# Optimization experiments

Measured on AMD Instinct MI355X. Metric: run time of the kernel, lower is better.

## Reference

```python
import jax, jax.numpy as jnp
import numpy as np

EPS = 1e-8

def _cdist(a, b):
    # Euclidean pairwise distances, torch.cdist(p=2) equivalent.
    sq = (jnp.sum(a * a, axis=1)[:, None] + jnp.sum(b * b, axis=1)[None, :]
          - 2.0 * (a @ b.T))
    return jnp.sqrt(jnp.maximum(sq, 1e-12))

def setup_inputs() -> dict:
    key = jax.random.key(0)
    k1, k2, k3, k4, k5, k6 = jax.random.split(key, 6)
    ns, n_cls, n_feat, K = 4096, 500, 256, 400
    return {
        "src_x": jax.random.normal(k1, (ns, n_feat), dtype=jnp.float32),
        "tgt_x": jax.random.normal(k2, (ns, n_feat), dtype=jnp.float32),
        "src_y": jax.random.uniform(k3, (ns, n_cls), dtype=jnp.float32),
        "tgt_y": jax.random.uniform(k4, (ns, n_cls), dtype=jnp.float32),
        "queue": jax.random.normal(k5, (n_cls, n_feat, K), dtype=jnp.float32),
        "queue_size": jax.random.randint(k6, (n_cls,), 0, K, dtype=jnp.int32),
    }

def reference(src_x, tgt_x, src_y, tgt_y, queue, queue_size):
    n_cls, n_feat, K = queue.shape
    num = queue_size.astype(queue.dtype)[:, None]                      # (C,1)
    # src_centroid: masked mean over the first queue_size[c] columns
    valid = (jnp.arange(K)[None, :] < queue_size[:, None]).astype(queue.dtype)  # (C,K)
    centroid = jnp.einsum('cfk,ck->cf', queue, valid) / jnp.maximum(num, 1.0)
    centroid = jnp.where(num > 0, centroid, 0.0)                       # (C,F)

    batch_src = src_y.T @ src_x                                        # (C,F)
    total_num = num + jnp.sum(src_y, axis=0)[:, None] + EPS            # (C,1)
    mean_src = (centroid * num + batch_src) / total_num                # (C,F)

    batch_prob = jnp.sum(tgt_y, axis=0)[:, None] + EPS                 # (C,1)
    mean_tgt = (tgt_y.T @ tgt_x) / batch_prob                          # (C,F)

    intra = jnp.diagonal(_cdist(mean_src, mean_tgt)).mean()
    inter = _cdist(mean_src, mean_src).mean()
    return intra, inter
```

## Files before the change

kernel.cpp:

```cpp
#include <hip/hip_runtime.h>
#include <math.h>

#define NS 4096
#define NC 500
#define NF 256
#define NK 400
#define KC_GEMM 16
#define NQB 4000

__global__ __launch_bounds__(256, 4) void k_heavy(
    const float* __restrict__ Xs, const float* __restrict__ Ys, float* __restrict__ Ps,
    const float* __restrict__ Xt, const float* __restrict__ Yt, float* __restrict__ Pt,
    float* __restrict__ CSs, float* __restrict__ CSt,
    const float* __restrict__ queue, const int* __restrict__ qsize,
    float* __restrict__ qsum) {
  __shared__ float ytile[256][16];
  __shared__ float csbuf[256];
  const int b    = blockIdx.x;
  const int tid  = threadIdx.x;
  const int w    = tid >> 6;
  const int lane = tid & 63;
  const int hp   = b % 5;

  for (int it = 0; it < 5; ++it) {
    if (it == hp) {
      const int z  = b >> 9;
      const int kc = (b >> 5) & 15;
      const int c0 = (b & 31) * 16;
      const float* X = z ? Xt : Xs;
      const float* Y = z ? Yt : Ys;
      float*       P = z ? Pt : Ps;
      float*      CS = z ? CSt : CSs;
      const int n0   = kc * 256;
      const int cmax = (NC - c0 < 16) ? (NC - c0) : 16;

      float csum = 0.f;
      for (int i = tid; i < 256 * 16; i += 256) {
        int rr = i >> 4, cc = i & 15;
        float v = (cc < cmax) ? Y[(size_t)(n0 + rr) * NC + c0 + cc] : 0.f;
        ytile[rr][cc] = v;
        csum += v;
      }
      csbuf[tid] = csum;
      __syncthreads();

      float acc[16];
      #pragma unroll
      for (int j = 0; j < 16; ++j) acc[j] = 0.f;
      const float* Xp = X + (size_t)n0 * NF + tid;

      #pragma unroll 4
      for (int n = 0; n < 256; ++n) {
        float xv = Xp[(size_t)n * NF];
        float4 y0 = *reinterpret_cast<const float4*>(&ytile[n][0]);
        float4 y1 = *reinterpret_cast<const float4*>(&ytile[n][4]);
        float4 y2 = *reinterpret_cast<const float4*>(&ytile[n][8]);
        float4 y3 = *reinterpret_cast<const float4*>(&ytile[n][12]);
        acc[0]  = fmaf(y0.x, xv, acc[0]);  acc[1]  = fmaf(y0.y, xv, acc[1]);
        acc[2]  = fmaf(y0.z, xv, acc[2]);  acc[3]  = fmaf(y0.w, xv, acc[3]);
        acc[4]  = fmaf(y1.x, xv, acc[4]);  acc[5]  = fmaf(y1.y, xv, acc[5]);
        acc[6]  = fmaf(y1.z, xv, acc[6]);  acc[7]  = fmaf(y1.w, xv, acc[7]);
        acc[8]  = fmaf(y2.x, xv, acc[8]);  acc[9]  = fmaf(y2.y, xv, acc[9]);
        acc[10] = fmaf(y2.z, xv, acc[10]); acc[11] = fmaf(y2.w, xv, acc[11]);
        acc[12] = fmaf(y3.x, xv, acc[12]); acc[13] = fmaf(y3.y, xv, acc[13]);
        acc[14] = fmaf(y3.z, xv, acc[14]); acc[15] = fmaf(y3.w, xv, acc[15]);
      }

      if (tid < 16) {
        float t = 0.f;
        #pragma unroll
        for (int j = 0; j < 16; ++j) t += csbuf[tid + 16 * j];
        CS[kc * 512 + c0 + tid] = t;
      }

      #pragma unroll
      for (int j = 0; j < 16; ++j)
        if (j < cmax) P[((size_t)kc * NC + c0 + j) * NF + tid] = acc[j];
      __syncthreads();

    } else {
      const int j = it - (it > hp ? 1 : 0);
      const int q = j * 1024 + b;
      if (q < NQB) {
        const int r0 = q * 32 + w * 8;
        const int c  = r0 >> 8;
        const int qs = qsize[c];
        const int L  = (qs + 3) >> 2;
        const float* base = queue + (size_t)r0 * NK;
        float s0 = 0.f, s1 = 0.f, s2 = 0.f, s3 = 0.f;
        float s4 = 0.f, s5 = 0.f, s6 = 0.f, s7 = 0.f;

        if (lane < L) {
          const int k = 4 * lane;
          float4 v0 = *reinterpret_cast<const float4*>(base + 0 * NK + k);
          float4 v1 = *reinterpret_cast<const float4*>(base + 1 * NK + k);
          float4 v2 = *reinterpret_cast<const float4*>(base + 2 * NK + k);
          float4 v3 = *reinterpret_cast<const float4*>(base + 3 * NK + k);
          float4 v4 = *reinterpret_cast<const float4*>(base + 4 * NK + k);
          float4 v5 = *reinterpret_cast<const float4*>(base + 5 * NK + k);
          float4 v6 = *reinterpret_cast<const float4*>(base + 6 * NK + k);
          float4 v7 = *reinterpret_cast<const float4*>(base + 7 * NK + k);
          s0 += v0.x; s1 += v1.x; s2 += v2.x; s3 += v3.x;
          s4 += v4.x; s5 += v5.x; s6 += v6.x; s7 += v7.x;
          if (k + 1 < qs) { s0 += v0.y; s1 += v1.y; s2 += v2.y; s3 += v3.y;
                            s4 += v4.y; s5 += v5.y; s6 += v6.y; s7 += v7.y; }
          if (k + 2 < qs) { s0 += v0.z; s1 += v1.z; s2 += v2.z; s3 += v3.z;
                            s4 += v4.z; s5 += v5.z; s6 += v6.z; s7 += v7.z; }
          if (k + 3 < qs) { s0 += v0.w; s1 += v1.w; s2 += v2.w; s3 += v3.w;
                            s4 += v4.w; s5 += v5.w; s6 += v6.w; s7 += v7.w; }
        }
        if (lane + 64 < L) {
          const int k = 256 + 4 * lane;
          float4 v0 = *reinterpret_cast<const float4*>(base + 0 * NK + k);
          float4 v1 = *reinterpret_cast<const float4*>(base + 1 * NK + k);
          float4 v2 = *reinterpret_cast<const float4*>(base + 2 * NK + k);
          float4 v3 = *reinterpret_cast<const float4*>(base + 3 * NK + k);
          float4 v4 = *reinterpret_cast<const float4*>(base + 4 * NK + k);
          float4 v5 = *reinterpret_cast<const float4*>(base + 5 * NK + k);
          float4 v6 = *reinterpret_cast<const float4*>(base + 6 * NK + k);
          float4 v7 = *reinterpret_cast<const float4*>(base + 7 * NK + k);
          s0 += v0.x; s1 += v1.x; s2 += v2.x; s3 += v3.x;
          s4 += v4.x; s5 += v5.x; s6 += v6.x; s7 += v7.x;
          if (k + 1 < qs) { s0 += v0.y; s1 += v1.y; s2 += v2.y; s3 += v3.y;
                            s4 += v4.y; s5 += v5.y; s6 += v6.y; s7 += v7.y; }
          if (k + 2 < qs) { s0 += v0.z; s1 += v1.z; s2 += v2.z; s3 += v3.z;
                            s4 += v4.z; s5 += v5.z; s6 += v6.z; s7 += v7.z; }
          if (k + 3 < qs) { s0 += v0.w; s1 += v1.w; s2 += v2.w; s3 += v3.w;
                            s4 += v4.w; s5 += v5.w; s6 += v6.w; s7 += v7.w; }
        }
        #pragma unroll
        for (int m = 32; m; m >>= 1) {
          s0 += __shfl_xor(s0, m); s1 += __shfl_xor(s1, m);
          s2 += __shfl_xor(s2, m); s3 += __shfl_xor(s3, m);
          s4 += __shfl_xor(s4, m); s5 += __shfl_xor(s5, m);
          s6 += __shfl_xor(s6, m); s7 += __shfl_xor(s7, m);
        }
        if (lane == 0) {
          *reinterpret_cast<float4*>(&qsum[r0])     = make_float4(s0, s1, s2, s3);
          *reinterpret_cast<float4*>(&qsum[r0 + 4]) = make_float4(s4, s5, s6, s7);
        }
      }
    }
  }
}

__global__ __launch_bounds__(256) void k_means(
    const float* __restrict__ qsum, const int* __restrict__ qsize,
    const float* __restrict__ Psrc, const float* __restrict__ Ptgt,
    const float* __restrict__ CSsrc, const float* __restrict__ CStgt,
    float* __restrict__ MS, float* __restrict__ MT, float* __restrict__ ipart) {
  const int c = blockIdx.x * 4 + (threadIdx.x >> 6);
  const int lane = threadIdx.x & 63;
  const int f4 = lane * 4;
  if (c >= NC) return;

  float cs_s = 0.f, cs_t = 0.f;
  #pragma unroll
  for (int kc = 0; kc < KC_GEMM; ++kc) {
    cs_s += CSsrc[kc * 512 + c];
    cs_t += CStgt[kc * 512 + c];
  }
  float num = (float)qsize[c];
  float4 ns = *reinterpret_cast<const float4*>(&qsum[(size_t)c * NF + f4]);
  float4 nt = make_float4(0.f, 0.f, 0.f, 0.f);
  #pragma unroll
  for (int kc = 0; kc < KC_GEMM; ++kc) {
    float4 ps = *reinterpret_cast<const float4*>(&Psrc[((size_t)kc * NC + c) * NF + f4]);
    float4 pt = *reinterpret_cast<const float4*>(&Ptgt[((size_t)kc * NC + c) * NF + f4]);
    ns.x += ps.x; ns.y += ps.y; ns.z += ps.z; ns.w += ps.w;
    nt.x += pt.x; nt.y += pt.y; nt.z += pt.z; nt.w += pt.w;
  }
  float rs = 1.f / (num + cs_s + 1e-8f);
  float rt = 1.f / (cs_t + 1e-8f);
  float4 ms = make_float4(ns.x * rs, ns.y * rs, ns.z * rs, ns.w * rs);
  float4 mt = make_float4(nt.x * rt, nt.y * rt, nt.z * rt, nt.w * rt);
  *reinterpret_cast<float4*>(&MS[(size_t)c * NF + f4]) = ms;
  *reinterpret_cast<float4*>(&MT[(size_t)c * NF + f4]) = mt;

  float dx = ms.x - mt.x, dy = ms.y - mt.y, dz = ms.z - mt.z, dw = ms.w - mt.w;
  float s = dx * dx + dy * dy + dz * dz + dw * dw;
  #pragma unroll
  for (int m = 32; m; m >>= 1) s += __shfl_xor(s, m);
  if (lane == 0) ipart[c] = sqrtf(fmaxf(s, 1e-12f));
}

#define TC 16
#define NBT 32
__global__ __launch_bounds__(256) void k_dist(const float* __restrict__ MS,
                                              float* __restrict__ epart) {
  __shared__ float a[TC][NF + 4];
  __shared__ float b[TC][NF + 4];
  const int bi = blockIdx.x & (NBT - 1);
  const int bj = blockIdx.x >> 5;

  for (int i = threadIdx.x; i < TC * (NF / 4); i += 256) {
    int rr = i >> 6, fq = (i & 63) * 4;
    int c1 = bi * TC + rr;
    int c2 = bj * TC + rr;
    float4 va = (c1 < NC) ? *reinterpret_cast<const float4*>(&MS[(size_t)c1 * NF + fq])
                          : make_float4(0.f, 0.f, 0.f, 0.f);
    float4 vb = (c2 < NC) ? *reinterpret_cast<const float4*>(&MS[(size_t)c2 * NF + fq])
                          : make_float4(0.f, 0.f, 0.f, 0.f);
    *reinterpret_cast<float4*>(&a[rr][fq]) = va;
    *reinterpret_cast<float4*>(&b[rr][fq]) = vb;
  }
  __syncthreads();

  const int i1 = threadIdx.x >> 4, i2 = threadIdx.x & 15;
  float s = 0.f;
  #pragma unroll 8
  for (int fq = 0; fq < NF; fq += 4) {
    float4 va = *reinterpret_cast<const float4*>(&a[i1][fq]);
    float4 vb = *reinterpret_cast<const float4*>(&b[i2][fq]);
    float d0 = va.x - vb.x, d1 = va.y - vb.y, d2 = va.z - vb.z, d3 = va.w - vb.w;
    s = fmaf(d0, d0, s); s = fmaf(d1, d1, s); s = fmaf(d2, d2, s); s = fmaf(d3, d3, s);
  }
  bool valid = (bi * TC + i1 < NC) && (bj * TC + i2 < NC);
  float rr = valid ? sqrtf(fmaxf(s, 1e-12f)) : 0.f;

  #pragma unroll
  for (int m = 32; m; m >>= 1) rr += __shfl_xor(rr, m);
  __shared__ float red[4];
  int wid = threadIdx.x >> 6, lane = threadIdx.x & 63;
  if (lane == 0) red[wid] = rr;
  __syncthreads();
  if (threadIdx.x == 0) epart[blockIdx.x] = red[0] + red[1] + red[2] + red[3];
}

__global__ __launch_bounds__(1024) void k_final(const float* __restrict__ ipart,
                                                const float* __restrict__ epart,
                                                float* __restrict__ out) {
  const int t = threadIdx.x;
  float si = (t < NC) ? ipart[t] : 0.f;
  float se = epart[t];
  #pragma unroll
  for (int m = 32; m; m >>= 1) { si += __shfl_xor(si, m); se += __shfl_xor(se, m); }
  __shared__ float ri[16], re[16];
  int wid = t >> 6, lane = t & 63;
  if (lane == 0) { ri[wid] = si; re[wid] = se; }
  __syncthreads();
  if (t == 0) {
    float A = 0.f, B = 0.f;
    #pragma unroll
    for (int w2 = 0; w2 < 16; ++w2) { A += ri[w2]; B += re[w2]; }
    out[0] = A / (float)NC;
    out[1] = B / ((float)NC * (float)NC);
  }
}

extern "C" void kernel_launch(void* const* d_in, const int* in_sizes, int n_in,
                              void* d_out, int out_size, void* d_ws, size_t ws_size,
                              hipStream_t stream) {
  const float* src_x = (const float*)d_in[0];
  const float* tgt_x = (const float*)d_in[1];
  const float* src_y = (const float*)d_in[2];
  const float* tgt_y = (const float*)d_in[3];
  const float* queue = (const float*)d_in[4];
  const int*   qsize = (const int*)d_in[5];
  float* out = (float*)d_out;

  float* ws    = (float*)d_ws;
  float* qsum  = ws;
  float* Psrc  = qsum + NC * NF;
  float* Ptgt  = Psrc + (size_t)KC_GEMM * NC * NF;
  float* CSs   = Ptgt + (size_t)KC_GEMM * NC * NF;
  float* CSt   = CSs + KC_GEMM * 512;
  float* MS    = CSt + KC_GEMM * 512;
  float* MT    = MS + NC * NF;
  float* ipart = MT + NC * NF;
  float* epart = ipart + NC;

  k_heavy<<<1024, 256, 0, stream>>>(
      src_x, src_y, Psrc, tgt_x, tgt_y, Ptgt, CSs, CSt, queue, qsize, qsum);

  k_means<<<(NC + 3) / 4, 256, 0, stream>>>(qsum, qsize, Psrc, Ptgt, CSs, CSt, MS, MT, ipart);

  k_dist<<<NBT * NBT, 256, 0, stream>>>(MS, epart);

  k_final<<<1, 1024, 0, stream>>>(ipart, epart, out);
}
```

Before: 83.53 us.

## Split heavy kernel into separate GEMM and queue-sum blocks, halve K-split

Replaces the persistent 1024-block interleaved schedule with one block per work item: 512 GEMM blocks that each cover 512 rows in two 256-row passes (K-split reduced from 16 to 8), followed by 4000 independent queue-reduction blocks. Halving the K-split cuts the partial-product writes and the reduction reads done later in k_means. The persistent loop and the occupancy hint are dropped in favour of hardware block scheduling. k_means now uses one block per class with scalar per-feature loads and a shared-memory reduction. The trade-off is less parallelism in the GEMM part and more block launches for the queue part.

```diff
diff --git a/kernel.cpp b/kernel.cpp
--- a/kernel.cpp
+++ b/kernel.cpp
@@ -5,10 +5,11 @@
 #define NC 500
 #define NF 256
 #define NK 400
-#define KC_GEMM 16
+#define KC_GEMM 8
+#define NB_GEMM (KC_GEMM * 32 * 2)
 #define NQB 4000
 
-__global__ __launch_bounds__(256, 4) void k_heavy(
+__global__ __launch_bounds__(256) void k_heavy(
     const float* __restrict__ Xs, const float* __restrict__ Ys, float* __restrict__ Ps,
     const float* __restrict__ Xt, const float* __restrict__ Yt, float* __restrict__ Pt,
     float* __restrict__ CSs, float* __restrict__ CSt,
@@ -16,39 +17,42 @@
     float* __restrict__ qsum) {
   __shared__ float ytile[256][16];
   __shared__ float csbuf[256];
-  const int b    = blockIdx.x;
+  const int bid  = blockIdx.x;
   const int tid  = threadIdx.x;
   const int w    = tid >> 6;
   const int lane = tid & 63;
-  const int hp   = b % 5;
-
-  for (int it = 0; it < 5; ++it) {
-    if (it == hp) {
-      const int z  = b >> 9;
-      const int kc = (b >> 5) & 15;
-      const int c0 = (b & 31) * 16;
-      const float* X = z ? Xt : Xs;
-      const float* Y = z ? Yt : Ys;
-      float*       P = z ? Pt : Ps;
-      float*      CS = z ? CSt : CSs;
-      const int n0   = kc * 256;
-      const int cmax = (NC - c0 < 16) ? (NC - c0) : 16;
-
-      float csum = 0.f;
-      for (int i = tid; i < 256 * 16; i += 256) {
-        int rr = i >> 4, cc = i & 15;
-        float v = (cc < cmax) ? Y[(size_t)(n0 + rr) * NC + c0 + cc] : 0.f;
-        ytile[rr][cc] = v;
-        csum += v;
+
+  if (bid < NB_GEMM) {
+    const int z   = bid >> 8;
+    const int rem = bid & 255;
+    const int kc  = rem >> 5;
+    const int c0  = (rem & 31) * 16;
+    const float* X = z ? Xt : Xs;
+    const float* Y = z ? Yt : Ys;
+    float*       P = z ? Pt : Ps;
+    float*      CS = z ? CSt : CSs;
+    const int n0   = kc * 512;
+    const int cmax = (NC - c0 < 16) ? (NC - c0) : 16;
+
+    float acc[16];
+    #pragma unroll
+    for (int j = 0; j < 16; ++j) acc[j] = 0.f;
+    float csum = 0.f;
+
+    for (int p = 0; p < 2; ++p) {
+      {
+        const int rr = tid >> 4, cc = tid & 15;
+        #pragma unroll
+        for (int j = 0; j < 16; ++j) {
+          float v = (cc < cmax)
+              ? Y[(size_t)(n0 + p * 256 + rr + 16 * j) * NC + c0 + cc] : 0.f;
+          ytile[rr + 16 * j][cc] = v;
+          csum += v;
+        }
       }
-      csbuf[tid] = csum;
       __syncthreads();
 
-      float acc[16];
-      #pragma unroll
-      for (int j = 0; j < 16; ++j) acc[j] = 0.f;
-      const float* Xp = X + (size_t)n0 * NF + tid;
-
+      const float* Xp = X + (size_t)(n0 + p * 256) * NF + tid;
       #pragma unroll 4
       for (int n = 0; n < 256; ++n) {
         float xv = Xp[(size_t)n * NF];
@@ -65,81 +69,80 @@
         acc[12] = fmaf(y3.x, xv, acc[12]); acc[13] = fmaf(y3.y, xv, acc[13]);
         acc[14] = fmaf(y3.z, xv, acc[14]); acc[15] = fmaf(y3.w, xv, acc[15]);
       }
-
-      if (tid < 16) {
-        float t = 0.f;
-        #pragma unroll
-        for (int j = 0; j < 16; ++j) t += csbuf[tid + 16 * j];
-        CS[kc * 512 + c0 + tid] = t;
-      }
-
+      __syncthreads();
+    }
+
+    csbuf[tid] = csum;
+    __syncthreads();
+    if (tid < 16) {
+      float t = 0.f;
       #pragma unroll
-      for (int j = 0; j < 16; ++j)
-        if (j < cmax) P[((size_t)kc * NC + c0 + j) * NF + tid] = acc[j];
-      __syncthreads();
-
-    } else {
-      const int j = it - (it > hp ? 1 : 0);
-      const int q = j * 1024 + b;
-      if (q < NQB) {
-        const int r0 = q * 32 + w * 8;
-        const int c  = r0 >> 8;
-        const int qs = qsize[c];
-        const int L  = (qs + 3) >> 2;
-        const float* base = queue + (size_t)r0 * NK;
-        float s0 = 0.f, s1 = 0.f, s2 = 0.f, s3 = 0.f;
-        float s4 = 0.f, s5 = 0.f, s6 = 0.f, s7 = 0.f;
-
-        if (lane < L) {
-          const int k = 4 * lane;
-          float4 v0 = *reinterpret_cast<const float4*>(base + 0 * NK + k);
-          float4 v1 = *reinterpret_cast<const float4*>(base + 1 * NK + k);
-          float4 v2 = *reinterpret_cast<const float4*>(base + 2 * NK + k);
-          float4 v3 = *reinterpret_cast<const float4*>(base + 3 * NK + k);
-          float4 v4 = *reinterpret_cast<const float4*>(base + 4 * NK + k);
-          float4 v5 = *reinterpret_cast<const float4*>(base + 5 * NK + k);
-          float4 v6 = *reinterpret_cast<const float4*>(base + 6 * NK + k);
-          float4 v7 = *reinterpret_cast<const float4*>(base + 7 * NK + k);
-          s0 += v0.x; s1 += v1.x; s2 += v2.x; s3 += v3.x;
-          s4 += v4.x; s5 += v5.x; s6 += v6.x; s7 += v7.x;
-          if (k + 1 < qs) { s0 += v0.y; s1 += v1.y; s2 += v2.y; s3 += v3.y;
-                            s4 += v4.y; s5 += v5.y; s6 += v6.y; s7 += v7.y; }
-          if (k + 2 < qs) { s0 += v0.z; s1 += v1.z; s2 += v2.z; s3 += v3.z;
-                            s4 += v4.z; s5 += v5.z; s6 += v6.z; s7 += v7.z; }
-          if (k + 3 < qs) { s0 += v0.w; s1 += v1.w; s2 += v2.w; s3 += v3.w;
-                            s4 += v4.w; s5 += v5.w; s6 += v6.w; s7 += v7.w; }
-        }
-        if (lane + 64 < L) {
-          const int k = 256 + 4 * lane;
-          float4 v0 = *reinterpret_cast<const float4*>(base + 0 * NK + k);
-          float4 v1 = *reinterpret_cast<const float4*>(base + 1 * NK + k);
-          float4 v2 = *reinterpret_cast<const float4*>(base + 2 * NK + k);
-          float4 v3 = *reinterpret_cast<const float4*>(base + 3 * NK + k);
-          float4 v4 = *reinterpret_cast<const float4*>(base + 4 * NK + k);
-          float4 v5 = *reinterpret_cast<const float4*>(base + 5 * NK + k);
-          float4 v6 = *reinterpret_cast<const float4*>(base + 6 * NK + k);
-          float4 v7 = *reinterpret_cast<const float4*>(base + 7 * NK + k);
-          s0 += v0.x; s1 += v1.x; s2 += v2.x; s3 += v3.x;
-          s4 += v4.x; s5 += v5.x; s6 += v6.x; s7 += v7.x;
-          if (k + 1 < qs) { s0 += v0.y; s1 += v1.y; s2 += v2.y; s3 += v3.y;
-                            s4 += v4.y; s5 += v5.y; s6 += v6.y; s7 += v7.y; }
-          if (k + 2 < qs) { s0 += v0.z; s1 += v1.z; s2 += v2.z; s3 += v3.z;
-                            s4 += v4.z; s5 += v5.z; s6 += v6.z; s7 += v7.z; }
-          if (k + 3 < qs) { s0 += v0.w; s1 += v1.w; s2 += v2.w; s3 += v3.w;
-                            s4 += v4.w; s5 += v5.w; s6 += v6.w; s7 += v7.w; }
-        }
-        #pragma unroll
-        for (int m = 32; m; m >>= 1) {
-          s0 += __shfl_xor(s0, m); s1 += __shfl_xor(s1, m);
-          s2 += __shfl_xor(s2, m); s3 += __shfl_xor(s3, m);
-          s4 += __shfl_xor(s4, m); s5 += __shfl_xor(s5, m);
-          s6 += __shfl_xor(s6, m); s7 += __shfl_xor(s7, m);
-        }
-        if (lane == 0) {
-          *reinterpret_cast<float4*>(&qsum[r0])     = make_float4(s0, s1, s2, s3);
-          *reinterpret_cast<float4*>(&qsum[r0 + 4]) = make_float4(s4, s5, s6, s7);
-        }
-      }
+      for (int j = 0; j < 16; ++j) t += csbuf[tid + 16 * j];
+      CS[kc * 512 + c0 + tid] = t;
+    }
+
+    #pragma unroll
+    for (int j = 0; j < 16; ++j)
+      if (j < cmax) P[((size_t)kc * NC + c0 + j) * NF + tid] = acc[j];
+
+  } else {
+    const int qb = bid - NB_GEMM;
+    const int r0 = (qb * 4 + w) * 8;
+    const int c  = r0 >> 8;
+    const int qs = qsize[c];
+    const int L  = (qs + 3) >> 2;
+    const float* base = queue + (size_t)r0 * NK;
+    float s0 = 0.f, s1 = 0.f, s2 = 0.f, s3 = 0.f;
+    float s4 = 0.f, s5 = 0.f, s6 = 0.f, s7 = 0.f;
+
+    if (lane < L) {
+      const int k = 4 * lane;
+      float4 v0 = *reinterpret_cast<const float4*>(base + 0 * NK + k);
+      float4 v1 = *reinterpret_cast<const float4*>(base + 1 * NK + k);
+      float4 v2 = *reinterpret_cast<const float4*>(base + 2 * NK + k);
+      float4 v3 = *reinterpret_cast<const float4*>(base + 3 * NK + k);
+      float4 v4 = *reinterpret_cast<const float4*>(base + 4 * NK + k);
+      float4 v5 = *reinterpret_cast<const float4*>(base + 5 * NK + k);
+      float4 v6 = *reinterpret_cast<const float4*>(base + 6 * NK + k);
+      float4 v7 = *reinterpret_cast<const float4*>(base + 7 * NK + k);
+      s0 += v0.x; s1 += v1.x; s2 += v2.x; s3 += v3.x;
+      s4 += v4.x; s5 += v5.x; s6 += v6.x; s7 += v7.x;
+      if (k + 1 < qs) { s0 += v0.y; s1 += v1.y; s2 += v2.y; s3 += v3.y;
+                        s4 += v4.y; s5 += v5.y; s6 += v6.y; s7 += v7.y; }
+      if (k + 2 < qs) { s0 += v0.z; s1 += v1.z; s2 += v2.z; s3 += v3.z;
+                        s4 += v4.z; s5 += v5.z; s6 += v6.z; s7 += v7.z; }
+      if (k + 3 < qs) { s0 += v0.w; s1 += v1.w; s2 += v2.w; s3 += v3.w;
+                        s4 += v4.w; s5 += v5.w; s6 += v6.w; s7 += v7.w; }
+    }
+    if (lane + 64 < L) {
+      const int k = 256 + 4 * lane;
+      float4 v0 = *reinterpret_cast<const float4*>(base + 0 * NK + k);
+      float4 v1 = *reinterpret_cast<const float4*>(base + 1 * NK + k);
+      float4 v2 = *reinterpret_cast<const float4*>(base + 2 * NK + k);
+      float4 v3 = *reinterpret_cast<const float4*>(base + 3 * NK + k);
+      float4 v4 = *reinterpret_cast<const float4*>(base + 4 * NK + k);
+      float4 v5 = *reinterpret_cast<const float4*>(base + 5 * NK + k);
+      float4 v6 = *reinterpret_cast<const float4*>(base + 6 * NK + k);
+      float4 v7 = *reinterpret_cast<const float4*>(base + 7 * NK + k);
+      s0 += v0.x; s1 += v1.x; s2 += v2.x; s3 += v3.x;
+      s4 += v4.x; s5 += v5.x; s6 += v6.x; s7 += v7.x;
+      if (k + 1 < qs) { s0 += v0.y; s1 += v1.y; s2 += v2.y; s3 += v3.y;
+                        s4 += v4.y; s5 += v5.y; s6 += v6.y; s7 += v7.y; }
+      if (k + 2 < qs) { s0 += v0.z; s1 += v1.z; s2 += v2.z; s3 += v3.z;
+                        s4 += v4.z; s5 += v5.z; s6 += v6.z; s7 += v7.z; }
+      if (k + 3 < qs) { s0 += v0.w; s1 += v1.w; s2 += v2.w; s3 += v3.w;
+                        s4 += v4.w; s5 += v5.w; s6 += v6.w; s7 += v7.w; }
+    }
+    #pragma unroll
+    for (int m = 32; m; m >>= 1) {
+      s0 += __shfl_xor(s0, m); s1 += __shfl_xor(s1, m);
+      s2 += __shfl_xor(s2, m); s3 += __shfl_xor(s3, m);
+      s4 += __shfl_xor(s4, m); s5 += __shfl_xor(s5, m);
+      s6 += __shfl_xor(s6, m); s7 += __shfl_xor(s7, m);
+    }
+    if (lane == 0) {
+      *reinterpret_cast<float4*>(&qsum[r0])     = make_float4(s0, s1, s2, s3);
+      *reinterpret_cast<float4*>(&qsum[r0 + 4]) = make_float4(s4, s5, s6, s7);
     }
   }
 }
@@ -149,10 +152,8 @@
     const float* __restrict__ Psrc, const float* __restrict__ Ptgt,
     const float* __restrict__ CSsrc, const float* __restrict__ CStgt,
     float* __restrict__ MS, float* __restrict__ MT, float* __restrict__ ipart) {
-  const int c = blockIdx.x * 4 + (threadIdx.x >> 6);
-  const int lane = threadIdx.x & 63;
-  const int f4 = lane * 4;
-  if (c >= NC) return;
+  const int c = blockIdx.x;
+  const int f = threadIdx.x;
 
   float cs_s = 0.f, cs_t = 0.f;
   #pragma unroll
@@ -161,27 +162,27 @@
     cs_t += CStgt[kc * 512 + c];
   }
   float num = (float)qsize[c];
-  float4 ns = *reinterpret_cast<const float4*>(&qsum[(size_t)c * NF + f4]);
-  float4 nt = make_float4(0.f, 0.f, 0.f, 0.f);
+  float ns = qsum[(size_t)c * NF + f];
+  float nt = 0.f;
   #pragma unroll
   for (int kc = 0; kc < KC_GEMM; ++kc) {
-    float4 ps = *reinterpret_cast<const float4*>(&Psrc[((size_t)kc * NC + c) * NF + f4]);
-    float4 pt = *reinterpret_cast<const float4*>(&Ptgt[((size_t)kc * NC + c) * NF + f4]);
-    ns.x += ps.x; ns.y += ps.y; ns.z += ps.z; ns.w += ps.w;
-    nt.x += pt.x; nt.y += pt.y; nt.z += pt.z; nt.w += pt.w;
-  }
-  float rs = 1.f / (num + cs_s + 1e-8f);
-  float rt = 1.f / (cs_t + 1e-8f);
-  float4 ms = make_float4(ns.x * rs, ns.y * rs, ns.z * rs, ns.w * rs);
-  float4 mt = make_float4(nt.x * rt, nt.y * rt, nt.z * rt, nt.w * rt);
-  *reinterpret_cast<float4*>(&MS[(size_t)c * NF + f4]) = ms;
-  *reinterpret_cast<float4*>(&MT[(size_t)c * NF + f4]) = mt;
-
-  float dx = ms.x - mt.x, dy = ms.y - mt.y, dz = ms.z - mt.z, dw = ms.w - mt.w;
-  float s = dx * dx + dy * dy + dz * dz + dw * dw;
+    ns += Psrc[((size_t)kc * NC + c) * NF + f];
+    nt += Ptgt[((size_t)kc * NC + c) * NF + f];
+  }
+  float ms = ns / (num + cs_s + 1e-8f);
+  float mt = nt / (cs_t + 1e-8f);
+  MS[(size_t)c * NF + f] = ms;
+  MT[(size_t)c * NF + f] = mt;
+
+  float d = ms - mt;
+  float s = d * d;
   #pragma unroll
   for (int m = 32; m; m >>= 1) s += __shfl_xor(s, m);
-  if (lane == 0) ipart[c] = sqrtf(fmaxf(s, 1e-12f));
+  __shared__ float red[4];
+  int wid = f >> 6, lane = f & 63;
+  if (lane == 0) red[wid] = s;
+  __syncthreads();
+  if (f == 0) ipart[c] = sqrtf(fmaxf(red[0] + red[1] + red[2] + red[3], 1e-12f));
 }
 
 #define TC 16
@@ -270,10 +271,10 @@
   float* ipart = MT + NC * NF;
   float* epart = ipart + NC;
 
-  k_heavy<<<1024, 256, 0, stream>>>(
+  k_heavy<<<NB_GEMM + NQB, 256, 0, stream>>>(
       src_x, src_y, Psrc, tgt_x, tgt_y, Ptgt, CSs, CSt, queue, qsize, qsum);
 
-  k_means<<<(NC + 3) / 4, 256, 0, stream>>>(qsum, qsize, Psrc, Ptgt, CSs, CSt, MS, MT, ipart);
+  k_means<<<NC, 256, 0, stream>>>(qsum, qsize, Psrc, Ptgt, CSs, CSt, MS, MT, ipart);
 
   k_dist<<<NBT * NBT, 256, 0, stream>>>(MS, epart);
 
```

Result: no change. 82.85 us (-0.8%).
